# Kernel optimization log

Hardware: AMD Instinct MI355X
Metric: run time of the kernel (lower is better)

The kernel has to match this reference:

```python
import jax, jax.numpy as jnp
import numpy as np

B, E, S = 2, 1024, 2048
H = 16
D_QK = D_V = D_OUT = 1024
NEG = -1e4


def setup_inputs() -> dict:
    key = jax.random.key(0)
    ks = jax.random.split(key, 12)
    q = jax.random.normal(ks[0], (B, E, 1, S), jnp.float32)
    k = jax.random.normal(ks[1], (B, E, 1, S), jnp.float32)
    v = jax.random.normal(ks[2], (B, E, 1, S), jnp.float32)
    # causal qk_mask: (B, src, 1, tgt); src index > tgt index is masked
    causal = jnp.where(jnp.arange(S)[:, None] > jnp.arange(S)[None, :], NEG, 0.0).astype(jnp.float32)
    qk_mask = jnp.broadcast_to(causal[None, :, None, :], (B, S, 1, S))
    k_mask = jnp.zeros((B, S, 1, 1), jnp.float32)
    sc = 1.0 / np.sqrt(E)
    Wq = jax.random.normal(ks[3], (D_QK, E), jnp.float32) * sc
    Wk = jax.random.normal(ks[4], (D_QK, E), jnp.float32) * sc
    Wv = jax.random.normal(ks[5], (D_V, E), jnp.float32) * sc
    Wo = jax.random.normal(ks[6], (D_OUT, D_V), jnp.float32) * sc
    bq = jnp.zeros((D_QK,), jnp.float32)
    bk = jnp.zeros((D_QK,), jnp.float32)
    bv = jnp.zeros((D_V,), jnp.float32)
    bo = jnp.zeros((D_OUT,), jnp.float32)
    return {"q": q, "k": k, "v": v, "qk_mask": qk_mask, "k_mask": k_mask,
            "Wq": Wq, "bq": bq, "Wk": Wk, "bk": bk, "Wv": Wv, "bv": bv,
            "Wo": Wo, "bo": bo}


def reference(q, k, v, qk_mask, k_mask, Wq, bq, Wk, bk, Wv, bv, Wo, bo):
    b, _, _, tq = q.shape
    sk = k.shape[3]
    d_qk, d_v = Wq.shape[0], Wv.shape[0]
    dh, dvh = d_qk // H, d_v // H
    fact = float(dh) ** (-0.5)
    # 1x1 conv projections on (B, C, 1, S) == matmul over channels
    qp = jnp.einsum('oc,bcis->bois', Wq, q) + bq[None, :, None, None]
    kp = jnp.einsum('oc,bcis->bois', Wk, k) + bk[None, :, None, None]
    vp = jnp.einsum('oc,bcis->bois', Wv, v) + bv[None, :, None, None]
    # split heads: channel dim is head-major (contiguous chunks)
    qh = qp[:, :, 0, :].reshape(b, H, dh, tq)
    kh = kp[:, :, 0, :].reshape(b, H, dh, sk)
    vh = vp[:, :, 0, :].reshape(b, H, dvh, sk)
    # scores: (B, H, src, tgt); masks broadcast over heads
    scores = jnp.einsum('bhcq,bhck->bhkq', qh, kh) * fact
    scores = scores + qk_mask[:, None, :, 0, :] + k_mask[:, None, :, 0, 0][..., None]
    w = jax.nn.softmax(scores, axis=2)  # softmax over src (k) axis
    attn = jnp.einsum('bhkq,bhck->bhcq', w, vh).reshape(b, d_v, 1, tq)
    out = jnp.einsum('oc,bcis->bois', Wo, attn) + bo[None, :, None, None]
    return out
```

## Files before the change

kernel.cpp:

```cpp
#include <hip/hip_runtime.h>
#include <hip/hip_bf16.h>
#include <stdint.h>

typedef unsigned short u16;
typedef __attribute__((ext_vector_type(8))) short short8;
typedef __attribute__((ext_vector_type(4))) short short4v;
typedef __attribute__((ext_vector_type(4))) float f32x4;

#define MFMA16(a,b,c) __builtin_amdgcn_mfma_f32_16x16x32_bf16((a),(b),(c),0,0,0)
#define EXP2F(x) __builtin_amdgcn_exp2f(x)

typedef const __attribute__((address_space(1))) void glb_void;
typedef __attribute__((address_space(3))) void lds_void;

__device__ __forceinline__ u16 f2b(float f){
  unsigned u = __float_as_uint(f);
  u += 0x7fffu + ((u>>16)&1u);
  return (u16)(u>>16);
}
__device__ __forceinline__ unsigned pack_bf16(float a, float b){
  __hip_bfloat162 h = __float22bfloat162_rn(make_float2(a,b));
  unsigned u; __builtin_memcpy(&u, &h, 4); return u;
}
__device__ __forceinline__ void gld16(const void* g, void* l){
  __builtin_amdgcn_global_load_lds((glb_void*)g, (lds_void*)l, 16, 0, 0);
}

__device__ __forceinline__ void stage128x64_sw(const u16* g, u16* lds, int gstride, int w, int lane){
  const int sub = lane>>3, c16 = lane&7;
  const int gcol = (c16 ^ sub)<<3;
  #pragma unroll
  for (int i=0;i<4;++i){
    int r0 = (w*4+i)*8;
    gld16(g + (size_t)(r0 + sub)*gstride + gcol, lds + r0*64);
  }
}
__device__ __forceinline__ void stage64x64_sw(const u16* g, u16* lds, int gstride, int w, int lane){
  const int sub = lane>>3, c16 = lane&7;
  const int gcol = (c16 ^ sub)<<3;
  #pragma unroll
  for (int i=0;i<2;++i){
    int r0 = (w*2+i)*8;
    gld16(g + (size_t)(r0 + sub)*gstride + gcol, lds + r0*64);
  }
}
__device__ __forceinline__ const short8* frag64(const u16* lds, int row, int c16){
  return (const short8*)(lds + row*64 + ((c16 ^ (row&7))<<3));
}
__device__ __forceinline__ void stage64x128_sw(const u16* g, u16* lds, int gstride, int w, int lane){
  const int sub = lane>>4, c16 = lane&15;
  #pragma unroll
  for (int i=0;i<4;++i){
    int r0 = (w*4+i)*4;
    int row = r0 + sub;
    gld16(g + (size_t)row*gstride + ((c16 ^ (row&15))<<3), lds + r0*128);
  }
}
__device__ __forceinline__ const short8* frag128(const u16* lds, int row, int c16){
  return (const short8*)(lds + row*128 + ((c16 ^ (row&15))<<3));
}

__global__ __launch_bounds__(256) void prep(
    const float* __restrict__ q, const float* __restrict__ k, const float* __restrict__ v,
    const float* __restrict__ qkm, const float* __restrict__ km,
    const float* __restrict__ Wq, const float* __restrict__ Wk,
    const float* __restrict__ Wv, const float* __restrict__ Wo,
    u16* __restrict__ W16, char* __restrict__ classes,
    u16* __restrict__ qT, u16* __restrict__ kT, u16* __restrict__ vT)
{
  __shared__ __align__(16) float t[64][72];
  const int bx = blockIdx.x, tid = threadIdx.x;
  const int S = 2048, E = 1024, nW = E*E;

  if (bx < 2048){
    const int sel = bx>>9, blk = bx&511;
    const float* src = sel==0?Wq : sel==1?Wk : sel==2?Wv : Wo;
    const float sc = (sel==0) ? 0.18033688f : 1.0f;
    u16* dst = W16 + (size_t)sel*nW;
    int i = (blk*256 + tid)*8;
    float4 a = *(const float4*)(src+i);
    float4 b = *(const float4*)(src+i+4);
    short8 o;
    o[0]=(short)f2b(a.x*sc); o[1]=(short)f2b(a.y*sc); o[2]=(short)f2b(a.z*sc); o[3]=(short)f2b(a.w*sc);
    o[4]=(short)f2b(b.x*sc); o[5]=(short)f2b(b.y*sc); o[6]=(short)f2b(b.z*sc); o[7]=(short)f2b(b.w*sc);
    *(short8*)(dst+i) = o;
  } else if (bx < 4096){
    const int tt = bx - 2048;
    const int b = tt>>10, qi = (tt>>5)&31, ki = tt&31;
    const int k0 = ki*64, q0 = qi*64;
    int az = 1, an = 1;
    #pragma unroll
    for (int p=0;p<4;++p){
      int e = tid + p*256;
      int row = e>>4, c4 = (e&15)*4;
      float kmv = km[(size_t)b*S + k0 + row];
      float4 mv = *(const float4*)&qkm[((size_t)b*S + k0 + row)*S + q0 + c4];
      mv.x += kmv; mv.y += kmv; mv.z += kmv; mv.w += kmv;
      az &= (mv.x==0.f) & (mv.y==0.f) & (mv.z==0.f) & (mv.w==0.f);
      an &= (mv.x<-1e3f) & (mv.y<-1e3f) & (mv.z<-1e3f) & (mv.w<-1e3f);
    }
    const int az_all = __syncthreads_and(az);
    const int an_all = __syncthreads_and(an);
    if (tid==0)
      classes[((size_t)b*32 + qi)*32 + ki] = an_all ? 2 : (az_all ? 0 : 1);
  } else {
    const int tt = bx - 4096;
    const int tensor = tt>>10, r = tt&1023;
    const int b = r>>9, rr = r&511;
    const int c0 = (rr>>5)*64, s0 = (rr&31)*64;
    const float* x = tensor==0 ? q : tensor==1 ? k : v;
    u16* xt = tensor==0 ? qT : tensor==1 ? kT : vT;
    #pragma unroll
    for (int p=0;p<4;++p){
      int e = tid + p*256;
      int row = e>>4, c4 = (e&15)*4;
      *(float4*)&t[row][c4] = *(const float4*)&x[((size_t)b*E + c0 + row)*S + s0 + c4];
    }
    __syncthreads();
    #pragma unroll
    for (int p=0;p<2;++p){
      int e = tid + p*256;
      int row = e>>3, col8 = (e&7)*8;
      short8 o;
      #pragma unroll
      for (int u=0;u<8;++u) o[u] = (short)f2b(t[col8+u][row]);
      *(short8*)&xt[((size_t)b*S + s0 + row)*E + c0 + col8] = o;
    }
  }
}

template<bool F32OUT>
__device__ __forceinline__ void gemm_core(
    const u16* __restrict__ A, const u16* __restrict__ Bt, const float* __restrict__ bias,
    float bscale, void* __restrict__ Cv, size_t cbase, int N, int K, int bias_on_m,
    int m0, int n0, u16* As, u16* Bs)
{
  const int tid = threadIdx.x, w = tid>>6, lane = tid&63;
  const int ln = lane&15, quad = lane>>4;
  const int m0w = (w>>1)*64, n0w = (w&1)*64;
  f32x4 acc[4][4];
  #pragma unroll
  for(int i=0;i<4;++i)
    #pragma unroll
    for(int j=0;j<4;++j) acc[i][j] = f32x4{0.f,0.f,0.f,0.f};

  for (int kc=0; kc<K; kc+=64){
    __syncthreads();
    stage128x64_sw(A  + (size_t)m0*K + kc, As, K, w, lane);
    stage128x64_sw(Bt + (size_t)n0*K + kc, Bs, K, w, lane);
    __syncthreads();
    #pragma unroll
    for (int kk=0; kk<64; kk+=32){
      const int c16 = (kk>>3) + quad;
      short8 af[4], bf[4];
      #pragma unroll
      for (int mt=0;mt<4;++mt) af[mt] = *frag64(As, m0w+mt*16+ln, c16);
      #pragma unroll
      for (int nt=0;nt<4;++nt) bf[nt] = *frag64(Bs, n0w+nt*16+ln, c16);
      #pragma unroll
      for (int mt=0;mt<4;++mt)
        #pragma unroll
        for (int nt=0;nt<4;++nt)
          acc[mt][nt] = MFMA16(af[mt], bf[nt], acc[mt][nt]);
    }
  }
  #pragma unroll
  for (int mt=0;mt<4;++mt){
    #pragma unroll
    for (int nt=0;nt<4;++nt){
      const int col = n0 + n0w + nt*16 + ln;
      const float bn = bias_on_m ? 0.f : bias[col]*bscale;
      #pragma unroll
      for (int r=0;r<4;++r){
        const int row = m0 + m0w + mt*16 + quad*4 + r;
        const float bb = bias_on_m ? bias[row]*bscale : bn;
        const float val = acc[mt][nt][r] + bb;
        const size_t idx = cbase + (size_t)row*N + col;
        if (F32OUT) ((float*)Cv)[idx] = val;
        else        ((u16*)Cv)[idx]   = f2b(val);
      }
    }
  }
}

__global__ __launch_bounds__(256,3) void proj(
    const u16* __restrict__ qT, const u16* __restrict__ kT, const u16* __restrict__ vT,
    const u16* __restrict__ W16,
    const float* __restrict__ bq, const float* __restrict__ bk, const float* __restrict__ bv,
    u16* __restrict__ Qb, u16* __restrict__ Kb, u16* __restrict__ Vb)
{
  __shared__ __align__(16) u16 As[128*64];
  __shared__ __align__(16) u16 Bs[128*64];
  const int bx = blockIdx.x;
  const int zone = bx>>7, r = bx&127;
  const size_t sSE = (size_t)2048*1024;
  const int nW = 1024*1024;
  if (zone < 4){
    const int sel = zone>>1, b = zone&1;
    const int m0 = (r>>3)*128, n0 = (r&7)*128;
    gemm_core<false>((sel? kT : qT) + b*sSE, W16 + (size_t)sel*nW, sel? bk : bq,
                     sel? 1.0f : 0.18033688f, sel? Kb : Qb, b*sSE,
                     1024, 1024, 0, m0, n0, As, Bs);
  } else {
    const int b = zone&1;
    const int m0 = (r>>4)*128, n0 = (r&15)*128;
    gemm_core<false>(W16 + (size_t)2*nW, vT + b*sSE, bv,
                     1.0f, Vb, b*sSE,
                     2048, 1024, 1, m0, n0, As, Bs);
  }
}

__global__ __launch_bounds__(256,4) void gemm_out64(
    const u16* __restrict__ Wo16, const u16* __restrict__ At, const float* __restrict__ bo,
    float* __restrict__ out)
{
  __shared__ __align__(16) u16 As[64*64];
  __shared__ __align__(16) u16 Bs[128*64];
  const int b = blockIdx.z;
  const int m0 = blockIdx.y*64, n0 = blockIdx.x*128;
  const size_t sSE = (size_t)2048*1024;
  const int K = 1024, N = 2048;
  const u16* Bt = At + b*sSE;
  const int tid = threadIdx.x, w = tid>>6, lane = tid&63;
  const int ln = lane&15, quad = lane>>4;
  const int m0w = (w>>1)*32, n0w = (w&1)*64;
  f32x4 acc[2][4];
  #pragma unroll
  for(int i=0;i<2;++i)
    #pragma unroll
    for(int j=0;j<4;++j) acc[i][j] = f32x4{0.f,0.f,0.f,0.f};

  for (int kc=0; kc<K; kc+=64){
    __syncthreads();
    stage64x64_sw (Wo16 + (size_t)m0*K + kc, As, K, w, lane);
    stage128x64_sw(Bt   + (size_t)n0*K + kc, Bs, K, w, lane);
    __syncthreads();
    #pragma unroll
    for (int kk=0; kk<64; kk+=32){
      const int c16 = (kk>>3) + quad;
      short8 af[2], bf[4];
      #pragma unroll
      for (int mt=0;mt<2;++mt) af[mt] = *frag64(As, m0w+mt*16+ln, c16);
      #pragma unroll
      for (int nt=0;nt<4;++nt) bf[nt] = *frag64(Bs, n0w+nt*16+ln, c16);
      #pragma unroll
      for (int mt=0;mt<2;++mt)
        #pragma unroll
        for (int nt=0;nt<4;++nt)
          acc[mt][nt] = MFMA16(af[mt], bf[nt], acc[mt][nt]);
    }
  }
  #pragma unroll
  for (int mt=0;mt<2;++mt){
    #pragma unroll
    for (int nt=0;nt<4;++nt){
      const int col = n0 + n0w + nt*16 + ln;
      #pragma unroll
      for (int r=0;r<4;++r){
        const int row = m0 + m0w + mt*16 + quad*4 + r;
        out[b*sSE + (size_t)row*N + col] = acc[mt][nt][r] + bo[row];
      }
    }
  }
}

__global__ __launch_bounds__(256,2) void attn(
    const u16* __restrict__ Qb, const u16* __restrict__ Kb, const u16* __restrict__ Vb,
    const float* __restrict__ qk_mask, const float* __restrict__ k_mask,
    const char* __restrict__ classes, u16* __restrict__ Ot)
{
  __shared__ __align__(16) u16 Ks[128*64];
  __shared__ __align__(16) u16 Vs[64*128];
  const int x = blockIdx.x;
  const int b = x&1, h = (x>>1)&15;
  const int pp = x>>5, pair = pp>>1, half = pp&1;
  const int tid = threadIdx.x, w = tid>>6, lane = tid&63;
  const int ln = lane&15, quad = lane>>4;
  const int S = 2048;
  const float LOG2E = 1.44269504f, C2 = 16.0f;

  #pragma unroll
  for (int sub=0; sub<2; ++sub){
    const int qt = sub ? pair : (15-pair);
    const int qbase = qt*128 + half*64;
    const int qg = qbase + w*16 + ln;
    short8 qf[2];
    #pragma unroll
    for (int kkI=0;kkI<2;++kkI)
      qf[kkI] = *(const short8*)&Qb[((size_t)b*S + qg)*1024 + h*64 + kkI*32 + quad*8];

    const char* cl = classes + ((size_t)b*32 + qt*2 + half)*32;
    float rs = 0.f;
    f32x4 acc[4];
    #pragma unroll
    for (int ct=0;ct<4;++ct) acc[ct] = f32x4{0.f,0.f,0.f,0.f};

    for (int kt=0; kt<16; ++kt){
      const char c0 = cl[2*kt], c1 = cl[2*kt+1];
      if (c0==2 && c1==2) continue;
      const bool nomask = (c0|c1)==0;
      const int k0 = kt*128;
      __syncthreads();
      stage128x64_sw(Kb + ((size_t)b*S + k0)*1024 + h*64, Ks, 1024, w, lane);
      stage64x128_sw(Vb + ((size_t)b*1024 + h*64)*S + k0, Vs, S, w, lane);
      __syncthreads();

      unsigned pk[8][2];
      #pragma unroll
      for (int t=0;t<8;++t){
        f32x4 s = f32x4{0.f,0.f,0.f,0.f};
        #pragma unroll
        for (int kkI=0;kkI<2;++kkI)
          s = MFMA16(*frag64(Ks, t*16+ln, kkI*4 + quad), qf[kkI], s);
        float e[4];
        if (nomask){
          #pragma unroll
          for (int r=0;r<4;++r) e[r] = EXP2F(s[r] - C2);
        } else {
          #pragma unroll
          for (int r=0;r<4;++r){
            const int kg = k0 + t*16 + quad*4 + r;
            const float m = qk_mask[((size_t)b*S + kg)*S + qg] + k_mask[(size_t)b*S + kg];
            e[r] = EXP2F(fmaf(m, LOG2E, s[r]) - C2);
          }
        }
        rs += (e[0]+e[1]) + (e[2]+e[3]);
        pk[t][0] = pack_bf16(e[0], e[1]);
        pk[t][1] = pack_bf16(e[2], e[3]);
      }
      const int srcA = (quad&1)*32 + ln, srcB = srcA + 16;
      const bool hi = (quad>>1)&1;
      #pragma unroll
      for (int c=0;c<4;++c){
        unsigned a0 = __shfl((int)pk[2*c][0],   srcA, 64);
        unsigned a1 = __shfl((int)pk[2*c][1],   srcA, 64);
        unsigned a2 = __shfl((int)pk[2*c][0],   srcB, 64);
        unsigned a3 = __shfl((int)pk[2*c][1],   srcB, 64);
        unsigned b0 = __shfl((int)pk[2*c+1][0], srcA, 64);
        unsigned b1 = __shfl((int)pk[2*c+1][1], srcA, 64);
        unsigned b2 = __shfl((int)pk[2*c+1][0], srcB, 64);
        unsigned b3 = __shfl((int)pk[2*c+1][1], srcB, 64);
        short8 pf;
        ((unsigned*)&pf)[0] = hi ? b0 : a0;
        ((unsigned*)&pf)[1] = hi ? b1 : a1;
        ((unsigned*)&pf)[2] = hi ? b2 : a2;
        ((unsigned*)&pf)[3] = hi ? b3 : a3;
        #pragma unroll
        for (int ct=0;ct<4;++ct)
          acc[ct] = MFMA16(*frag128(Vs, ct*16+ln, c*4 + quad), pf, acc[ct]);
      }
    }
    rs += __shfl_xor(rs, 16, 64);
    rs += __shfl_xor(rs, 32, 64);
    const float rinv = 1.0f / rs;
    #pragma unroll
    for (int ct=0;ct<4;++ct){
      short4v o4;
      #pragma unroll
      for (int r=0;r<4;++r) o4[r] = (short)f2b(acc[ct][r] * rinv);
      *(short4v*)&Ot[((size_t)b*S + qg)*1024 + h*64 + ct*16 + quad*4] = o4;
    }
  }
}

extern "C" void kernel_launch(void* const* d_in, const int* in_sizes, int n_in,
                              void* d_out, int out_size, void* d_ws, size_t ws_size,
                              hipStream_t stream)
{
  const float* q   = (const float*)d_in[0];
  const float* k   = (const float*)d_in[1];
  const float* v   = (const float*)d_in[2];
  const float* qkm = (const float*)d_in[3];
  const float* km  = (const float*)d_in[4];
  const float* Wq  = (const float*)d_in[5];
  const float* bq  = (const float*)d_in[6];
  const float* Wk  = (const float*)d_in[7];
  const float* bk  = (const float*)d_in[8];
  const float* Wv  = (const float*)d_in[9];
  const float* bv  = (const float*)d_in[10];
  const float* Wo  = (const float*)d_in[11];
  const float* bo  = (const float*)d_in[12];
  float* out = (float*)d_out;

  const size_t nAct = (size_t)2*2048*1024;
  const int   nW   = 1024*1024;

  u16* A0 = (u16*)d_ws;
  u16* A1 = A0 + nAct;
  u16* A2 = A1 + nAct;
  u16* A3 = A2 + nAct;
  u16* A4 = A3 + nAct;
  u16* A5 = A4 + nAct;
  u16* W16 = A5 + nAct;
  char* classes = (char*)(W16 + (size_t)4*nW);
  u16* Wo16 = W16 + (size_t)3*nW;

  dim3 blk(256);
  prep      <<<dim3(7168), blk, 0, stream>>>(q, k, v, qkm, km, Wq, Wk, Wv, Wo,
                                             W16, classes, A0, A1, A2);
  proj      <<<dim3(768),  blk, 0, stream>>>(A0, A1, A2, W16, bq, bk, bv, A3, A4, A5);
  attn      <<<dim3(512),  blk, 0, stream>>>(A3, A4, A5, qkm, km, classes, A0);
  gemm_out64<<<dim3(16,16,2), blk, 0, stream>>>(Wo16, A0, bo, out);
}
```

Baseline: 260.7 us.

## Merge paired query tiles into one KV sweep with register-prefetched staging

The attention kernel now processes both paired causal query tiles in a single pass over the union of needed key tiles, so each K/V tile is loaded once and shared by both. Instead of direct global-to-LDS loads with two syncs per tile, the next tile is prefetched into registers while the current one is computed, then written to LDS. The PV MFMA block is also raised in wave priority. This cuts K/V traffic and hides load latency, at the cost of doubled accumulators and extra register pressure that may hurt occupancy under launch_bounds(256,2).

```diff
diff --git a/kernel.cpp b/kernel.cpp
--- a/kernel.cpp
+++ b/kernel.cpp
@@ -46,15 +46,6 @@
 }
 __device__ __forceinline__ const short8* frag64(const u16* lds, int row, int c16){
   return (const short8*)(lds + row*64 + ((c16 ^ (row&7))<<3));
-}
-__device__ __forceinline__ void stage64x128_sw(const u16* g, u16* lds, int gstride, int w, int lane){
-  const int sub = lane>>4, c16 = lane&15;
-  #pragma unroll
-  for (int i=0;i<4;++i){
-    int r0 = (w*4+i)*4;
-    int row = r0 + sub;
-    gld16(g + (size_t)row*gstride + ((c16 ^ (row&15))<<3), lds + r0*128);
-  }
 }
 __device__ __forceinline__ const short8* frag128(const u16* lds, int row, int c16){
   return (const short8*)(lds + row*128 + ((c16 ^ (row&15))<<3));
@@ -279,77 +270,129 @@
   const int S = 2048;
   const float LOG2E = 1.44269504f, C2 = 16.0f;
 
-  #pragma unroll
-  for (int sub=0; sub<2; ++sub){
-    const int qt = sub ? pair : (15-pair);
-    const int qbase = qt*128 + half*64;
-    const int qg = qbase + w*16 + ln;
-    short8 qf[2];
-    #pragma unroll
-    for (int kkI=0;kkI<2;++kkI)
-      qf[kkI] = *(const short8*)&Qb[((size_t)b*S + qg)*1024 + h*64 + kkI*32 + quad*8];
-
-    const char* cl = classes + ((size_t)b*32 + qt*2 + half)*32;
-    float rs = 0.f;
-    f32x4 acc[4];
-    #pragma unroll
-    for (int ct=0;ct<4;++ct) acc[ct] = f32x4{0.f,0.f,0.f,0.f};
-
-    for (int kt=0; kt<16; ++kt){
-      const char c0 = cl[2*kt], c1 = cl[2*kt+1];
-      if (c0==2 && c1==2) continue;
-      const bool nomask = (c0|c1)==0;
-      const int k0 = kt*128;
-      __syncthreads();
-      stage128x64_sw(Kb + ((size_t)b*S + k0)*1024 + h*64, Ks, 1024, w, lane);
-      stage64x128_sw(Vb + ((size_t)b*1024 + h*64)*S + k0, Vs, S, w, lane);
-      __syncthreads();
-
-      unsigned pk[8][2];
-      #pragma unroll
-      for (int t=0;t<8;++t){
-        f32x4 s = f32x4{0.f,0.f,0.f,0.f};
+  const int qtA = 15-pair, qtB = pair;
+  const int qgA = qtA*128 + half*64 + w*16 + ln;
+  const int qgB = qtB*128 + half*64 + w*16 + ln;
+  short8 qfA[2], qfB[2];
+  #pragma unroll
+  for (int kkI=0;kkI<2;++kkI){
+    qfA[kkI] = *(const short8*)&Qb[((size_t)b*S + qgA)*1024 + h*64 + kkI*32 + quad*8];
+    qfB[kkI] = *(const short8*)&Qb[((size_t)b*S + qgB)*1024 + h*64 + kkI*32 + quad*8];
+  }
+  const char* clA = classes + ((size_t)b*32 + qtA*2 + half)*32;
+  const char* clB = classes + ((size_t)b*32 + qtB*2 + half)*32;
+
+  unsigned mA=0, mB=0;
+  #pragma unroll
+  for (int kt=0;kt<16;++kt){
+    if (!((clA[2*kt]==2) & (clA[2*kt+1]==2))) mA |= 1u<<kt;
+    if (!((clB[2*kt]==2) & (clB[2*kt+1]==2))) mB |= 1u<<kt;
+  }
+  const unsigned mS = mA|mB;
+
+  float rsA=0.f, rsB=0.f;
+  f32x4 accA[4], accB[4];
+  #pragma unroll
+  for (int ct=0;ct<4;++ct){ accA[ct]=f32x4{0.f,0.f,0.f,0.f}; accB[ct]=f32x4{0.f,0.f,0.f,0.f}; }
+
+  const u16* gK = Kb + ((size_t)b*S)*1024 + h*64;
+  const u16* gV = Vb + ((size_t)b*1024 + h*64)*S;
+  const int subK = lane>>3, cK = ((lane&7)^subK)<<3;
+  const int subV = lane>>4, cV0 = lane&15;
+
+  short8 kreg[4], vreg[4];
+  auto issue = [&](int kt){
+    const int k0 = kt*128;
+    #pragma unroll
+    for (int i=0;i<4;++i){
+      const int r = (w*4+i)*8 + subK;
+      kreg[i] = *(const short8*)(gK + (size_t)(k0 + r)*1024 + cK);
+    }
+    #pragma unroll
+    for (int i=0;i<4;++i){
+      const int row = (w*4+i)*4 + subV;
+      vreg[i] = *(const short8*)(gV + (size_t)row*S + k0 + ((cV0 ^ (row&15))<<3));
+    }
+  };
+  auto write_lds = [&](){
+    #pragma unroll
+    for (int i=0;i<4;++i)
+      *(short8*)&Ks[(w*4+i)*512 + lane*8] = kreg[i];
+    #pragma unroll
+    for (int i=0;i<4;++i)
+      *(short8*)&Vs[(w*4+i)*512 + lane*8] = vreg[i];
+  };
+
+  auto compute = [&](const short8* qf, const char* cl, int kt, int qg, float& rs, f32x4* acc){
+    const char c0 = cl[2*kt], c1 = cl[2*kt+1];
+    const bool nomask = (c0|c1)==0;
+    const int k0 = kt*128;
+    unsigned pk[8][2];
+    #pragma unroll
+    for (int t=0;t<8;++t){
+      f32x4 s = f32x4{0.f,0.f,0.f,0.f};
+      #pragma unroll
+      for (int kkI=0;kkI<2;++kkI)
+        s = MFMA16(*frag64(Ks, t*16+ln, kkI*4 + quad), qf[kkI], s);
+      float e[4];
+      if (nomask){
         #pragma unroll
-        for (int kkI=0;kkI<2;++kkI)
-          s = MFMA16(*frag64(Ks, t*16+ln, kkI*4 + quad), qf[kkI], s);
-        float e[4];
-        if (nomask){
-          #pragma unroll
-          for (int r=0;r<4;++r) e[r] = EXP2F(s[r] - C2);
-        } else {
-          #pragma unroll
-          for (int r=0;r<4;++r){
-            const int kg = k0 + t*16 + quad*4 + r;
-            const float m = qk_mask[((size_t)b*S + kg)*S + qg] + k_mask[(size_t)b*S + kg];
-            e[r] = EXP2F(fmaf(m, LOG2E, s[r]) - C2);
-          }
+        for (int r=0;r<4;++r) e[r] = EXP2F(s[r] - C2);
+      } else {
+        #pragma unroll
+        for (int r=0;r<4;++r){
+          const int kg = k0 + t*16 + quad*4 + r;
+          const float m = qk_mask[((size_t)b*S + kg)*S + qg] + k_mask[(size_t)b*S + kg];
+          e[r] = EXP2F(fmaf(m, LOG2E, s[r]) - C2);
         }
-        rs += (e[0]+e[1]) + (e[2]+e[3]);
-        pk[t][0] = pack_bf16(e[0], e[1]);
-        pk[t][1] = pack_bf16(e[2], e[3]);
       }
-      const int srcA = (quad&1)*32 + ln, srcB = srcA + 16;
-      const bool hi = (quad>>1)&1;
-      #pragma unroll
-      for (int c=0;c<4;++c){
-        unsigned a0 = __shfl((int)pk[2*c][0],   srcA, 64);
-        unsigned a1 = __shfl((int)pk[2*c][1],   srcA, 64);
-        unsigned a2 = __shfl((int)pk[2*c][0],   srcB, 64);
-        unsigned a3 = __shfl((int)pk[2*c][1],   srcB, 64);
-        unsigned b0 = __shfl((int)pk[2*c+1][0], srcA, 64);
-        unsigned b1 = __shfl((int)pk[2*c+1][1], srcA, 64);
-        unsigned b2 = __shfl((int)pk[2*c+1][0], srcB, 64);
-        unsigned b3 = __shfl((int)pk[2*c+1][1], srcB, 64);
-        short8 pf;
-        ((unsigned*)&pf)[0] = hi ? b0 : a0;
-        ((unsigned*)&pf)[1] = hi ? b1 : a1;
-        ((unsigned*)&pf)[2] = hi ? b2 : a2;
-        ((unsigned*)&pf)[3] = hi ? b3 : a3;
-        #pragma unroll
-        for (int ct=0;ct<4;++ct)
-          acc[ct] = MFMA16(*frag128(Vs, ct*16+ln, c*4 + quad), pf, acc[ct]);
-      }
-    }
+      rs += (e[0]+e[1]) + (e[2]+e[3]);
+      pk[t][0] = pack_bf16(e[0], e[1]);
+      pk[t][1] = pack_bf16(e[2], e[3]);
+    }
+    const int srcA = (quad&1)*32 + ln, srcB = srcA + 16;
+    const bool hi = (quad>>1)&1;
+    #pragma unroll
+    for (int c=0;c<4;++c){
+      unsigned a0 = __shfl((int)pk[2*c][0],   srcA, 64);
+      unsigned a1 = __shfl((int)pk[2*c][1],   srcA, 64);
+      unsigned a2 = __shfl((int)pk[2*c][0],   srcB, 64);
+      unsigned a3 = __shfl((int)pk[2*c][1],   srcB, 64);
+      unsigned b0 = __shfl((int)pk[2*c+1][0], srcA, 64);
+      unsigned b1 = __shfl((int)pk[2*c+1][1], srcA, 64);
+      unsigned b2 = __shfl((int)pk[2*c+1][0], srcB, 64);
+      unsigned b3 = __shfl((int)pk[2*c+1][1], srcB, 64);
+      short8 pf;
+      ((unsigned*)&pf)[0] = hi ? b0 : a0;
+      ((unsigned*)&pf)[1] = hi ? b1 : a1;
+      ((unsigned*)&pf)[2] = hi ? b2 : a2;
+      ((unsigned*)&pf)[3] = hi ? b3 : a3;
+      __builtin_amdgcn_s_setprio(1);
+      #pragma unroll
+      for (int ct=0;ct<4;++ct)
+        acc[ct] = MFMA16(*frag128(Vs, ct*16+ln, c*4 + quad), pf, acc[ct]);
+      __builtin_amdgcn_s_setprio(0);
+    }
+  };
+
+  int cur = mS ? (__ffs(mS)-1) : 16;
+  if (cur < 16) issue(cur);
+  while (cur < 16){
+    const unsigned above = mS & (0xfffffffeu << cur);
+    const int nxt = above ? (__ffs(above)-1) : 16;
+    __builtin_amdgcn_s_barrier();
+    __builtin_amdgcn_sched_barrier(0);
+    write_lds();
+    if (nxt < 16) issue(nxt);
+    asm volatile("s_waitcnt lgkmcnt(0)" ::: "memory");
+    __builtin_amdgcn_s_barrier();
+    __builtin_amdgcn_sched_barrier(0);
+    if ((mA>>cur)&1) compute(qfA, clA, cur, qgA, rsA, accA);
+    if ((mB>>cur)&1) compute(qfB, clB, cur, qgB, rsB, accB);
+    cur = nxt;
+  }
+
+  auto epi = [&](float rs, f32x4* acc, int qg){
     rs += __shfl_xor(rs, 16, 64);
     rs += __shfl_xor(rs, 32, 64);
     const float rinv = 1.0f / rs;
@@ -360,7 +403,9 @@
       for (int r=0;r<4;++r) o4[r] = (short)f2b(acc[ct][r] * rinv);
       *(short4v*)&Ot[((size_t)b*S + qg)*1024 + h*64 + ct*16 + quad*4] = o4;
     }
-  }
+  };
+  epi(rsA, accA, qgA);
+  epi(rsB, accB, qgB);
 }
 
 extern "C" void kernel_launch(void* const* d_in, const int* in_sizes, int n_in,
```

Result: faster. 242.9 us (-6.8%).
